# Performance work log

Hardware: AMD Instinct MI355X
Metric: run time of the kernel (lower is better)

## Reference

```python
import jax, jax.numpy as jnp
import numpy as np

N, G, C, CV, H = 2, 8, 64, 64, 2048
KA_ITERS = 2
EPS = 1e-20


def setup_inputs() -> dict:
    key = jax.random.key(0)
    k1, k2, k3 = jax.random.split(key, 3)
    q = jax.random.normal(k1, (N, G, C, H), dtype=jnp.float32)
    zeta = jax.random.normal(k2, (N, G, C, H), dtype=jnp.float32)
    mu = jax.random.normal(k3, (N, G, CV, H), dtype=jnp.float32)
    alpha = jnp.full((1,), 1.0 / np.sqrt(C), dtype=jnp.float32)  # uniform query precision
    beta = jnp.full((1,), 0.05, dtype=jnp.float32)               # uniform value precision
    return {"q": q, "zeta": zeta, "alpha": alpha, "mu": mu, "beta": beta}


def reference(q, zeta, alpha, mu, beta):
    # q, zeta: [N,G,C,H]; mu: [N,G,Cv,H]; alpha, beta: scalar (shape [1])
    a = alpha[0]
    b = beta[0]
    q2 = jnp.sum(q * q, axis=-2)      # [N,G,H]
    mu2 = jnp.sum(mu * mu, axis=-2)   # [N,G,H]

    def update_weights(zeta):
        z2 = jnp.sum(zeta * zeta, axis=-2)                     # [N,G,H]
        qz = jnp.einsum('bgci,bgcj->bgij', q, zeta)            # [N,G,H,H]
        # -0.5*alpha*||q_i - zeta_j||^2 (Mahalanobis with uniform precision)
        logp = -0.5 * a * (q2[..., :, None] + z2[..., None, :] - 2.0 * qz)
        # magnitude priors: + 0.5*alpha*||zeta_j||^2 + 0.5*beta*||mu_j||^2
        logp = logp + 0.5 * a * z2[..., None, :] + 0.5 * b * mu2[..., None, :]
        m = jnp.max(logp, axis=-1, keepdims=True)
        w = jnp.exp(logp - m)
        w = w / (jnp.sum(w, axis=-1, keepdims=True) + EPS)
        return w

    w = update_weights(zeta)
    for _ in range(KA_ITERS):
        # key adaptation (no zeta prior): zeta_j = sum_i w_ij q_i / sum_i w_ij
        zeta_upd = jnp.einsum('bgij,bgci->bgcj', w, q)         # [N,G,C,H]
        sum_w = jnp.sum(w, axis=-2, keepdims=True)             # [N,G,1,H]
        zeta = zeta_upd / sum_w
        w = update_weights(zeta)

    # value update: v_i = sum_j w_ij mu_j
    return jnp.einsum('bgij,bgcj->bgci', w, mu)                # [N,G,Cv,H]
```

## Files before the change

### kernel.cpp

```cpp
#include <hip/hip_runtime.h>

#define NB 16
#define CD 64
#define HD 2048

typedef unsigned short u16;
typedef __attribute__((ext_vector_type(8))) short s16x8;
typedef __attribute__((ext_vector_type(4))) float f32x4;

__device__ __forceinline__ u16 f2bf(float x){
    unsigned u = __float_as_uint(x);
    u += 0x7FFFu + ((u >> 16) & 1u);
    return (u16)(u >> 16);
}
__device__ __forceinline__ float bf2f(u16 h){ return __uint_as_float(((unsigned)h) << 16); }
__device__ __forceinline__ void split2(float x, u16& h, u16& l){
    h = f2bf(x); l = f2bf(x - bf2f(h));
}
union Frag { uint4 q; s16x8 s; };
__device__ __forceinline__ s16x8 ld8(const u16* p){ Frag f; f.q = *(const uint4*)p; return f.s; }
__device__ __forceinline__ f32x4 mfma16(s16x8 a, s16x8 b, f32x4 c){
    return __builtin_amdgcn_mfma_f32_16x16x32_bf16(a, b, c, 0, 0, 0);
}
__device__ __forceinline__ f32x4 mm2(s16x8 ah, s16x8 al, s16x8 bh, f32x4 c){
    c = mfma16(ah, bh, c);
    c = mfma16(al, bh, c);
    return c;
}
__device__ __forceinline__ f32x4 z4(){ f32x4 v = {0.f,0.f,0.f,0.f}; return v; }

__device__ __forceinline__ void xcd_map(int& bg, int& tile){
    int lb = blockIdx.y*32 + blockIdx.x;
    int xcd = lb & 7, t = lb >> 3;
    bg = 2*xcd + (t >> 5);
    tile = t & 31;
}


__global__ void k_convert(const float* __restrict__ src, u16* __restrict__ dh,
                          u16* __restrict__ dl, int n4)
{
    int idx = blockIdx.x*256 + threadIdx.x;
    if (idx >= n4) return;
    float4 v = ((const float4*)src)[idx];
    ushort4 h, l;
    split2(v.x, h.x, l.x); split2(v.y, h.y, l.y);
    split2(v.z, h.z, l.z); split2(v.w, h.w, l.w);
    ((ushort4*)dh)[idx] = h;
    ((ushort4*)dl)[idx] = l;
}

__global__ void k_convert1(const float* __restrict__ src, u16* __restrict__ dh, int n4)
{
    int idx = blockIdx.x*256 + threadIdx.x;
    if (idx >= n4) return;
    float4 v = ((const float4*)src)[idx];
    ushort4 h;
    h.x = f2bf(v.x); h.y = f2bf(v.y); h.z = f2bf(v.z); h.w = f2bf(v.w);
    ((ushort4*)dh)[idx] = h;
}

__global__ void k_transpose1(const float* __restrict__ src, u16* __restrict__ dh)
{
    int bg = blockIdx.y, h0 = blockIdx.x*128, tid = threadIdx.x;
    __shared__ float ft[CD][132];
    #pragma unroll
    for (int k=0;k<8;k++){
        int flat = tid + 256*k;
        int c = flat >> 5, p = (flat & 31)*4;
        *(float4*)&ft[c][p] = *(const float4*)(src + ((size_t)bg*CD + c)*HD + h0 + p);
    }
    __syncthreads();
    int hl = tid >> 1, c0 = (tid & 1)*32;
    union { u16 u[32]; uint4 q[4]; } oh;
    #pragma unroll
    for (int m=0;m<32;m++)
        oh.u[m] = f2bf(ft[c0+m][hl]);
    size_t base = ((size_t)bg*HD + h0 + hl)*CD + c0;
    #pragma unroll
    for (int t=0;t<4;t++)
        *((uint4*)(dh + base) + t) = oh.q[t];
}

__global__ void k_bias(const float* __restrict__ mu, const float* __restrict__ beta,
                       float* __restrict__ bias)
{
    int bg = blockIdx.y;
    int j  = blockIdx.x*256 + threadIdx.x;
    const float* m = mu + (size_t)bg*CD*HD + j;
    float s = 0.f;
    #pragma unroll
    for (int c=0;c<CD;c++){ float v = m[(size_t)c*HD]; s = fmaf(v, v, s); }
    bias[(size_t)bg*HD + j] = 0.5f * beta[0] * s;
}


__global__ __launch_bounds__(256,2) void k_rowsum(
    const u16* __restrict__ qTh,
    const u16* __restrict__ zTh,
    const float* __restrict__ bias, const float* __restrict__ alpha,
    float* __restrict__ r)
{
    int bg, itile; xcd_map(bg, itile);
    const int i0 = itile*64;
    const int tid = threadIdx.x, wave = tid>>6, lane = tid&63, ln = lane&15, quad = lane>>4;
    const int jw = wave*32;
    const float a = alpha[0];
    __shared__ float rpart[4][64];

    s16x8 Ah[4][2];
    #pragma unroll
    for (int mt=0;mt<4;mt++)
        #pragma unroll
        for (int ks=0;ks<2;ks++){
            size_t off = ((size_t)bg*HD + i0 + mt*16 + ln)*CD + ks*32 + quad*8;
            Ah[mt][ks] = ld8(qTh + off);
        }
    float racc[16];
    #pragma unroll
    for (int k=0;k<16;k++) racc[k] = 0.f;
    const float* bb = bias + (size_t)bg*HD;

    s16x8 B0h[2][2], B1h[2][2];
    float bj0[2], bj1[2];

    #pragma unroll
    for (int nt=0;nt<2;nt++){
        #pragma unroll
        for (int ks=0;ks<2;ks++){
            size_t off = ((size_t)bg*HD + jw + nt*16 + ln)*CD + ks*32 + quad*8;
            B0h[nt][ks] = ld8(zTh + off);
        }
        bj0[nt] = bb[jw + nt*16 + ln];
    }

    for (int j0=0;j0<HD;j0+=256){
        #pragma unroll
        for (int nt=0;nt<2;nt++){
            #pragma unroll
            for (int ks=0;ks<2;ks++){
                size_t off = ((size_t)bg*HD + j0+128 + jw + nt*16 + ln)*CD + ks*32 + quad*8;
                B1h[nt][ks] = ld8(zTh + off);
            }
            bj1[nt] = bb[j0+128 + jw + nt*16 + ln];
        }
        __builtin_amdgcn_sched_barrier(0);
        {
            f32x4 acc[4][2];
            #pragma unroll
            for (int mt=0;mt<4;mt++){ acc[mt][0]=z4(); acc[mt][1]=z4(); }
            __builtin_amdgcn_s_setprio(1);
            #pragma unroll
            for (int ks=0;ks<2;ks++)
                #pragma unroll
                for (int mt=0;mt<4;mt++)
                    #pragma unroll
                    for (int nt=0;nt<2;nt++)
                        acc[mt][nt] = mfma16(Ah[mt][ks], B0h[nt][ks], acc[mt][nt]);
            __builtin_amdgcn_s_setprio(0);
            #pragma unroll
            for (int mt=0;mt<4;mt++)
                #pragma unroll
                for (int nt=0;nt<2;nt++)
                    #pragma unroll
                    for (int rx=0;rx<4;rx++)
                        racc[mt*4+rx] += __expf(fmaf(a, acc[mt][nt][rx], bj0[nt]));
        }
        {
            int jn2 = (j0+256) & (HD-1);
            #pragma unroll
            for (int nt=0;nt<2;nt++){
                #pragma unroll
                for (int ks=0;ks<2;ks++){
                    size_t off = ((size_t)bg*HD + jn2 + jw + nt*16 + ln)*CD + ks*32 + quad*8;
                    B0h[nt][ks] = ld8(zTh + off);
                }
                bj0[nt] = bb[jn2 + jw + nt*16 + ln];
            }
        }
        __builtin_amdgcn_sched_barrier(0);
        {
            f32x4 acc[4][2];
            #pragma unroll
            for (int mt=0;mt<4;mt++){ acc[mt][0]=z4(); acc[mt][1]=z4(); }
            __builtin_amdgcn_s_setprio(1);
            #pragma unroll
            for (int ks=0;ks<2;ks++)
                #pragma unroll
                for (int mt=0;mt<4;mt++)
                    #pragma unroll
                    for (int nt=0;nt<2;nt++)
                        acc[mt][nt] = mfma16(Ah[mt][ks], B1h[nt][ks], acc[mt][nt]);
            __builtin_amdgcn_s_setprio(0);
            #pragma unroll
            for (int mt=0;mt<4;mt++)
                #pragma unroll
                for (int nt=0;nt<2;nt++)
                    #pragma unroll
                    for (int rx=0;rx<4;rx++)
                        racc[mt*4+rx] += __expf(fmaf(a, acc[mt][nt][rx], bj1[nt]));
        }
    }
    #pragma unroll
    for (int k=0;k<16;k++){
        float v = racc[k];
        v += __shfl_xor(v,1); v += __shfl_xor(v,2);
        v += __shfl_xor(v,4); v += __shfl_xor(v,8);
        racc[k] = v;
    }
    if (ln == 0){
        #pragma unroll
        for (int mt=0;mt<4;mt++)
            #pragma unroll
            for (int rx=0;rx<4;rx++)
                rpart[wave][mt*16 + quad*4 + rx] = racc[mt*4+rx];
    }
    __syncthreads();
    if (tid < 64)
        r[(size_t)bg*HD + i0 + tid] = rpart[0][tid]+rpart[1][tid]+rpart[2][tid]+rpart[3][tid];
}

__global__ __launch_bounds__(256,2) void k_update(
    const u16* __restrict__ qTh,
    u16* zTh,
    const u16* __restrict__ qNh,
    const float* __restrict__ bias, const float* __restrict__ alpha,
    const float* __restrict__ r)
{
    int bg, jtile; xcd_map(bg, jtile);
    const int j0 = jtile*64;
    const int tid = threadIdx.x, wave = tid>>6, lane = tid&63, ln = lane&15, quad = lane>>4;
    const int cm = (wave&1)*32, jn = (wave>>1)*32;
    const float a = alpha[0];
    __shared__ u16 wl[2][64*128];
    __shared__ float denl[4][64];

    s16x8 Bh[4][2];
    #pragma unroll
    for (int nt=0;nt<4;nt++)
        #pragma unroll
        for (int ks=0;ks<2;ks++){
            size_t off = ((size_t)bg*HD + j0 + nt*16 + ln)*CD + ks*32 + quad*8;
            Bh[nt][ks] = ld8(zTh + off);
        }
    float bj[4];
    #pragma unroll
    for (int nt=0;nt<4;nt++) bj[nt] = bias[(size_t)bg*HD + j0 + nt*16 + ln];

    f32x4 acc2[2][2] = {{z4(),z4()},{z4(),z4()}};
    float den[4] = {0.f,0.f,0.f,0.f};
    int buf = 0;

    for (int is=0; is<HD; is+=128, buf^=1){
        s16x8 Ah[2][2];
        #pragma unroll
        for (int ks=0;ks<2;ks++)
            #pragma unroll
            for (int mt=0;mt<2;mt++){
                size_t off = ((size_t)bg*HD + is + wave*32 + mt*16 + ln)*CD + ks*32 + quad*8;
                Ah[mt][ks] = ld8(qTh + off);
            }
        s16x8 A2h[4][2];
        #pragma unroll
        for (int ks2=0;ks2<4;ks2++)
            #pragma unroll
            for (int mtN=0;mtN<2;mtN++){
                size_t off = ((size_t)bg*CD + cm + mtN*16 + ln)*HD + is + ks2*32 + quad*8;
                A2h[ks2][mtN] = ld8(qNh + off);
            }
        float ri[8];
        #pragma unroll
        for (int mt=0;mt<2;mt++){
            float4 rv = *(const float4*)&r[(size_t)bg*HD + is + wave*32 + mt*16 + quad*4];
            ri[mt*4+0] = __builtin_amdgcn_rcpf(rv.x);
            ri[mt*4+1] = __builtin_amdgcn_rcpf(rv.y);
            ri[mt*4+2] = __builtin_amdgcn_rcpf(rv.z);
            ri[mt*4+3] = __builtin_amdgcn_rcpf(rv.w);
        }
        __builtin_amdgcn_sched_barrier(0);
        f32x4 acc1[2][4];
        #pragma unroll
        for (int mt=0;mt<2;mt++)
            #pragma unroll
            for (int nt=0;nt<4;nt++) acc1[mt][nt] = z4();
        __builtin_amdgcn_s_setprio(1);
        #pragma unroll
        for (int ks=0;ks<2;ks++)
            #pragma unroll
            for (int mt=0;mt<2;mt++)
                #pragma unroll
                for (int nt=0;nt<4;nt++)
                    acc1[mt][nt] = mfma16(Ah[mt][ks], Bh[nt][ks], acc1[mt][nt]);
        __builtin_amdgcn_s_setprio(0);
        #pragma unroll
        for (int mt=0;mt<2;mt++)
            #pragma unroll
            for (int nt=0;nt<4;nt++){
                u16 hh[4];
                #pragma unroll
                for (int rx=0;rx<4;rx++){
                    float w = __expf(fmaf(a, acc1[mt][nt][rx], bj[nt])) * ri[mt*4+rx];
                    hh[rx] = f2bf(w);
                    den[nt] += bf2f(hh[rx]);
                }
                int row = nt*16 + ln;
                int c4  = wave*32 + mt*16 + quad*4;
                int off = (row<<7) + ((((c4>>3) ^ (row&15))<<3) | (c4&7));
                *(ushort4*)&wl[buf][off] = make_ushort4(hh[0],hh[1],hh[2],hh[3]);
            }
        __syncthreads();
        __builtin_amdgcn_s_setprio(1);
        #pragma unroll
        for (int ks2=0;ks2<4;ks2++){
            s16x8 B2h[2];
            #pragma unroll
            for (int nt2=0;nt2<2;nt2++){
                int jl = jn + nt2*16 + ln;
                int ob = (jl<<7) + (((ks2*4+quad) ^ (jl&15))<<3);
                B2h[nt2] = ld8(&wl[buf][ob]);
            }
            #pragma unroll
            for (int mtN=0;mtN<2;mtN++)
                #pragma unroll
                for (int nt2=0;nt2<2;nt2++)
                    acc2[mtN][nt2] = mfma16(A2h[ks2][mtN], B2h[nt2], acc2[mtN][nt2]);
        }
        __builtin_amdgcn_s_setprio(0);
    }
    #pragma unroll
    for (int nt=0;nt<4;nt++){
        float v = den[nt];
        v += __shfl_xor(v,16); v += __shfl_xor(v,32);
        if (quad == 0) denl[wave][nt*16 + ln] = v;
    }
    __syncthreads();
    #pragma unroll
    for (int nt2=0;nt2<2;nt2++){
        int jl = jn + nt2*16 + ln;
        float dinv = __builtin_amdgcn_rcpf(denl[0][jl]+denl[1][jl]+denl[2][jl]+denl[3][jl]);
        #pragma unroll
        for (int mtN=0;mtN<2;mtN++){
            u16 hh[4];
            #pragma unroll
            for (int rx=0;rx<4;rx++)
                hh[rx] = f2bf(acc2[mtN][nt2][rx] * dinv);
            size_t off = ((size_t)bg*HD + j0 + jl)*CD + cm + mtN*16 + quad*4;
            *(ushort4*)(zTh + off) = make_ushort4(hh[0],hh[1],hh[2],hh[3]);
        }
    }
}

__global__ __launch_bounds__(256,2) void k_final(
    const u16* __restrict__ qTh,
    const u16* __restrict__ zTh,
    const u16* __restrict__ muh, const u16* __restrict__ mul_,
    const float* __restrict__ bias, const float* __restrict__ alpha,
    float* __restrict__ out)
{
    int bg, itile; xcd_map(bg, itile);
    const int i0 = itile*64;
    const int tid = threadIdx.x, wave = tid>>6, lane = tid&63, ln = lane&15, quad = lane>>4;
    const int cm = (wave&1)*32, in_ = (wave>>1)*32;
    const float a = alpha[0];
    __shared__ u16 el[2][64*128];
    __shared__ float rl2[4][64];

    s16x8 Bh[4][2];
    #pragma unroll
    for (int nt=0;nt<4;nt++)
        #pragma unroll
        for (int ks=0;ks<2;ks++){
            size_t off = ((size_t)bg*HD + i0 + nt*16 + ln)*CD + ks*32 + quad*8;
            Bh[nt][ks] = ld8(qTh + off);
        }
    f32x4 acc2[2][2] = {{z4(),z4()},{z4(),z4()}};
    float racc[4] = {0.f,0.f,0.f,0.f};
    int buf = 0;

    for (int js=0; js<HD; js+=128, buf^=1){
        s16x8 Ah[2][2];
        #pragma unroll
        for (int ks=0;ks<2;ks++)
            #pragma unroll
            for (int mt=0;mt<2;mt++){
                size_t off = ((size_t)bg*HD + js + wave*32 + mt*16 + ln)*CD + ks*32 + quad*8;
                Ah[mt][ks] = ld8(zTh + off);
            }
        s16x8 A2h[4][2], A2l[4][2];
        #pragma unroll
        for (int ks2=0;ks2<4;ks2++)
            #pragma unroll
            for (int mtN=0;mtN<2;mtN++){
                size_t off = ((size_t)bg*CD + cm + mtN*16 + ln)*HD + js + ks2*32 + quad*8;
                A2h[ks2][mtN] = ld8(muh + off);
                A2l[ks2][mtN] = ld8(mul_ + off);
            }
        float bj8[8];
        #pragma unroll
        for (int mt=0;mt<2;mt++){
            float4 bv = *(const float4*)&bias[(size_t)bg*HD + js + wave*32 + mt*16 + quad*4];
            bj8[mt*4+0]=bv.x; bj8[mt*4+1]=bv.y; bj8[mt*4+2]=bv.z; bj8[mt*4+3]=bv.w;
        }
        __builtin_amdgcn_sched_barrier(0);
        f32x4 acc1[2][4];
        #pragma unroll
        for (int mt=0;mt<2;mt++)
            #pragma unroll
            for (int nt=0;nt<4;nt++) acc1[mt][nt] = z4();
        __builtin_amdgcn_s_setprio(1);
        #pragma unroll
        for (int ks=0;ks<2;ks++)
            #pragma unroll
            for (int mt=0;mt<2;mt++)
                #pragma unroll
                for (int nt=0;nt<4;nt++)
                    acc1[mt][nt] = mfma16(Ah[mt][ks], Bh[nt][ks], acc1[mt][nt]);
        __builtin_amdgcn_s_setprio(0);
        #pragma unroll
        for (int mt=0;mt<2;mt++)
            #pragma unroll
            for (int nt=0;nt<4;nt++){
                u16 hh[4];
                #pragma unroll
                for (int rx=0;rx<4;rx++){
                    float e = __expf(fmaf(a, acc1[mt][nt][rx], bj8[mt*4+rx]));
                    hh[rx] = f2bf(e);
                    racc[nt] += bf2f(hh[rx]);
                }
                int row = nt*16 + ln;
                int c4  = wave*32 + mt*16 + quad*4;
                int off = (row<<7) + ((((c4>>3) ^ (row&15))<<3) | (c4&7));
                *(ushort4*)&el[buf][off] = make_ushort4(hh[0],hh[1],hh[2],hh[3]);
            }
        __syncthreads();
        __builtin_amdgcn_s_setprio(1);
        #pragma unroll
        for (int ks2=0;ks2<4;ks2++){
            s16x8 B2h[2];
            #pragma unroll
            for (int nt2=0;nt2<2;nt2++){
                int il = in_ + nt2*16 + ln;
                int ob = (il<<7) + (((ks2*4+quad) ^ (il&15))<<3);
                B2h[nt2] = ld8(&el[buf][ob]);
            }
            #pragma unroll
            for (int mtN=0;mtN<2;mtN++)
                #pragma unroll
                for (int nt2=0;nt2<2;nt2++)
                    acc2[mtN][nt2] = mm2(A2h[ks2][mtN], A2l[ks2][mtN], B2h[nt2], acc2[mtN][nt2]);
        }
        __builtin_amdgcn_s_setprio(0);
    }
    #pragma unroll
    for (int nt=0;nt<4;nt++){
        float v = racc[nt];
        v += __shfl_xor(v,16); v += __shfl_xor(v,32);
        if (quad == 0) rl2[wave][nt*16 + ln] = v;
    }
    __syncthreads();
    #pragma unroll
    for (int nt2=0;nt2<2;nt2++){
        int il = in_ + nt2*16 + ln;
        float rinv = __builtin_amdgcn_rcpf(rl2[0][il]+rl2[1][il]+rl2[2][il]+rl2[3][il]);
        #pragma unroll
        for (int mtN=0;mtN<2;mtN++)
            #pragma unroll
            for (int rx=0;rx<4;rx++)
                out[((size_t)bg*CD + cm + mtN*16 + quad*4 + rx)*HD + i0 + il]
                    = acc2[mtN][nt2][rx] * rinv;
    }
}

extern "C" void kernel_launch(void* const* d_in, const int* in_sizes, int n_in,
                              void* d_out, int out_size, void* d_ws, size_t ws_size,
                              hipStream_t stream)
{
    (void)in_sizes; (void)n_in; (void)out_size; (void)ws_size;
    const float* q     = (const float*)d_in[0];
    const float* zeta  = (const float*)d_in[1];
    const float* alpha = (const float*)d_in[2];
    const float* mu    = (const float*)d_in[3];
    const float* beta  = (const float*)d_in[4];
    float* out = (float*)d_out;

    const size_t SZ = (size_t)NB*HD*CD;
    u16* qTh = (u16*)d_ws;
    u16* zTh = qTh + 1*SZ;
    u16* qNh = qTh + 2*SZ;
    u16* muh = qTh + 3*SZ;
    u16* mul_= qTh + 4*SZ;
    float* bias = (float*)(qTh + 5*SZ);
    float* r    = bias + (size_t)NB*HD;

    dim3 blk(256,1,1);
    int n4 = (int)(SZ/4);
    k_convert1 <<<dim3(n4/256), blk, 0, stream>>>(q,  qNh, n4);
    k_convert  <<<dim3(n4/256), blk, 0, stream>>>(mu, muh, mul_, n4);
    k_transpose1<<<dim3(HD/128, NB), blk, 0, stream>>>(q,    qTh);
    k_transpose1<<<dim3(HD/128, NB), blk, 0, stream>>>(zeta, zTh);
    k_bias     <<<dim3(HD/256, NB), blk, 0, stream>>>(mu, beta, bias);

    k_rowsum<<<dim3(HD/64, NB), blk, 0, stream>>>(qTh,zTh,bias,alpha,r);
    k_update<<<dim3(HD/64, NB), blk, 0, stream>>>(qTh,zTh,qNh,bias,alpha,r);
    k_rowsum<<<dim3(HD/64, NB), blk, 0, stream>>>(qTh,zTh,bias,alpha,r);
    k_update<<<dim3(HD/64, NB), blk, 0, stream>>>(qTh,zTh,qNh,bias,alpha,r);
    k_final <<<dim3(HD/64, NB), blk, 0, stream>>>(qTh,zTh,muh,mul_,bias,alpha,out);
}
```

Before: 333.9 us.

## Software-pipeline global loads in update/final kernels and fuse q prep kernels

The k_update and k_final main loops are unrolled by two with ping-pong register sets, so the next tile's q/zeta fragments, reciprocals and bias loads are issued right after the current tile's first MFMA batch. This lets global-load latency hide behind the exp and second-GEMM work, where before it was exposed at the top of each iteration. Separately, the bf16 conversion of q and its transpose are merged into one kernel so q is read from global memory once. The cost is higher register pressure from the duplicated fragment buffers, which could lower occupancy.

```diff
diff --git a/kernel.cpp b/kernel.cpp
--- a/kernel.cpp
+++ b/kernel.cpp
@@ -50,14 +50,32 @@
     ((ushort4*)dl)[idx] = l;
 }
 
-__global__ void k_convert1(const float* __restrict__ src, u16* __restrict__ dh, int n4)
+__global__ void k_prep_q(const float* __restrict__ src, u16* __restrict__ dT,
+                         u16* __restrict__ dN)
 {
-    int idx = blockIdx.x*256 + threadIdx.x;
-    if (idx >= n4) return;
-    float4 v = ((const float4*)src)[idx];
-    ushort4 h;
-    h.x = f2bf(v.x); h.y = f2bf(v.y); h.z = f2bf(v.z); h.w = f2bf(v.w);
-    ((ushort4*)dh)[idx] = h;
+    int bg = blockIdx.y, h0 = blockIdx.x*128, tid = threadIdx.x;
+    __shared__ float ft[CD][132];
+    #pragma unroll
+    for (int k=0;k<8;k++){
+        int flat = tid + 256*k;
+        int c = flat >> 5, p = (flat & 31)*4;
+        size_t goff = ((size_t)bg*CD + c)*HD + h0 + p;
+        float4 v = *(const float4*)(src + goff);
+        *(float4*)&ft[c][p] = v;
+        ushort4 h;
+        h.x = f2bf(v.x); h.y = f2bf(v.y); h.z = f2bf(v.z); h.w = f2bf(v.w);
+        *(ushort4*)(dN + goff) = h;
+    }
+    __syncthreads();
+    int hl = tid >> 1, c0 = (tid & 1)*32;
+    union { u16 u[32]; uint4 q[4]; } oh;
+    #pragma unroll
+    for (int m=0;m<32;m++)
+        oh.u[m] = f2bf(ft[c0+m][hl]);
+    size_t base = ((size_t)bg*HD + h0 + hl)*CD + c0;
+    #pragma unroll
+    for (int t=0;t<4;t++)
+        *((uint4*)(dT + base) + t) = oh.q[t];
 }
 
 __global__ void k_transpose1(const float* __restrict__ src, u16* __restrict__ dh)
@@ -249,83 +267,185 @@
 
     f32x4 acc2[2][2] = {{z4(),z4()},{z4(),z4()}};
     float den[4] = {0.f,0.f,0.f,0.f};
-    int buf = 0;
-
-    for (int is=0; is<HD; is+=128, buf^=1){
-        s16x8 Ah[2][2];
-        #pragma unroll
-        for (int ks=0;ks<2;ks++)
+
+    s16x8 Ah0[2][2], A2h0[4][2]; float ri0[8];
+    s16x8 Ah1[2][2], A2h1[4][2]; float ri1[8];
+
+    #pragma unroll
+    for (int ks=0;ks<2;ks++)
+        #pragma unroll
+        for (int mt=0;mt<2;mt++){
+            size_t off = ((size_t)bg*HD + 0 + wave*32 + mt*16 + ln)*CD + ks*32 + quad*8;
+            Ah0[mt][ks] = ld8(qTh + off);
+        }
+    #pragma unroll
+    for (int ks2=0;ks2<4;ks2++)
+        #pragma unroll
+        for (int mtN=0;mtN<2;mtN++){
+            size_t off = ((size_t)bg*CD + cm + mtN*16 + ln)*HD + 0 + ks2*32 + quad*8;
+            A2h0[ks2][mtN] = ld8(qNh + off);
+        }
+    #pragma unroll
+    for (int mt=0;mt<2;mt++){
+        float4 rv = *(const float4*)&r[(size_t)bg*HD + 0 + wave*32 + mt*16 + quad*4];
+        ri0[mt*4+0] = __builtin_amdgcn_rcpf(rv.x);
+        ri0[mt*4+1] = __builtin_amdgcn_rcpf(rv.y);
+        ri0[mt*4+2] = __builtin_amdgcn_rcpf(rv.z);
+        ri0[mt*4+3] = __builtin_amdgcn_rcpf(rv.w);
+    }
+
+    for (int t=0; t<16; t+=2){
+        const int is1 = (t+1)*128, is2 = (t+2)*128;
+
+        {
+            f32x4 acc1[2][4];
+            #pragma unroll
+            for (int mt=0;mt<2;mt++)
+                #pragma unroll
+                for (int nt=0;nt<4;nt++) acc1[mt][nt] = z4();
+            __builtin_amdgcn_s_setprio(1);
+            #pragma unroll
+            for (int ks=0;ks<2;ks++)
+                #pragma unroll
+                for (int mt=0;mt<2;mt++)
+                    #pragma unroll
+                    for (int nt=0;nt<4;nt++)
+                        acc1[mt][nt] = mfma16(Ah0[mt][ks], Bh[nt][ks], acc1[mt][nt]);
+            __builtin_amdgcn_s_setprio(0);
+            #pragma unroll
+            for (int ks=0;ks<2;ks++)
+                #pragma unroll
+                for (int mt=0;mt<2;mt++){
+                    size_t off = ((size_t)bg*HD + is1 + wave*32 + mt*16 + ln)*CD + ks*32 + quad*8;
+                    Ah1[mt][ks] = ld8(qTh + off);
+                }
+            #pragma unroll
+            for (int ks2=0;ks2<4;ks2++)
+                #pragma unroll
+                for (int mtN=0;mtN<2;mtN++){
+                    size_t off = ((size_t)bg*CD + cm + mtN*16 + ln)*HD + is1 + ks2*32 + quad*8;
+                    A2h1[ks2][mtN] = ld8(qNh + off);
+                }
             #pragma unroll
             for (int mt=0;mt<2;mt++){
-                size_t off = ((size_t)bg*HD + is + wave*32 + mt*16 + ln)*CD + ks*32 + quad*8;
-                Ah[mt][ks] = ld8(qTh + off);
-            }
-        s16x8 A2h[4][2];
-        #pragma unroll
-        for (int ks2=0;ks2<4;ks2++)
-            #pragma unroll
-            for (int mtN=0;mtN<2;mtN++){
-                size_t off = ((size_t)bg*CD + cm + mtN*16 + ln)*HD + is + ks2*32 + quad*8;
-                A2h[ks2][mtN] = ld8(qNh + off);
-            }
-        float ri[8];
-        #pragma unroll
-        for (int mt=0;mt<2;mt++){
-            float4 rv = *(const float4*)&r[(size_t)bg*HD + is + wave*32 + mt*16 + quad*4];
-            ri[mt*4+0] = __builtin_amdgcn_rcpf(rv.x);
-            ri[mt*4+1] = __builtin_amdgcn_rcpf(rv.y);
-            ri[mt*4+2] = __builtin_amdgcn_rcpf(rv.z);
-            ri[mt*4+3] = __builtin_amdgcn_rcpf(rv.w);
-        }
-        __builtin_amdgcn_sched_barrier(0);
-        f32x4 acc1[2][4];
-        #pragma unroll
-        for (int mt=0;mt<2;mt++)
-            #pragma unroll
-            for (int nt=0;nt<4;nt++) acc1[mt][nt] = z4();
-        __builtin_amdgcn_s_setprio(1);
-        #pragma unroll
-        for (int ks=0;ks<2;ks++)
+                float4 rv = *(const float4*)&r[(size_t)bg*HD + is1 + wave*32 + mt*16 + quad*4];
+                ri1[mt*4+0] = __builtin_amdgcn_rcpf(rv.x);
+                ri1[mt*4+1] = __builtin_amdgcn_rcpf(rv.y);
+                ri1[mt*4+2] = __builtin_amdgcn_rcpf(rv.z);
+                ri1[mt*4+3] = __builtin_amdgcn_rcpf(rv.w);
+            }
+            __builtin_amdgcn_sched_barrier(0);
             #pragma unroll
             for (int mt=0;mt<2;mt++)
                 #pragma unroll
-                for (int nt=0;nt<4;nt++)
-                    acc1[mt][nt] = mfma16(Ah[mt][ks], Bh[nt][ks], acc1[mt][nt]);
-        __builtin_amdgcn_s_setprio(0);
-        #pragma unroll
-        for (int mt=0;mt<2;mt++)
-            #pragma unroll
-            for (int nt=0;nt<4;nt++){
-                u16 hh[4];
-                #pragma unroll
-                for (int rx=0;rx<4;rx++){
-                    float w = __expf(fmaf(a, acc1[mt][nt][rx], bj[nt])) * ri[mt*4+rx];
-                    hh[rx] = f2bf(w);
-                    den[nt] += bf2f(hh[rx]);
-                }
-                int row = nt*16 + ln;
-                int c4  = wave*32 + mt*16 + quad*4;
-                int off = (row<<7) + ((((c4>>3) ^ (row&15))<<3) | (c4&7));
-                *(ushort4*)&wl[buf][off] = make_ushort4(hh[0],hh[1],hh[2],hh[3]);
-            }
-        __syncthreads();
-        __builtin_amdgcn_s_setprio(1);
-        #pragma unroll
-        for (int ks2=0;ks2<4;ks2++){
-            s16x8 B2h[2];
-            #pragma unroll
-            for (int nt2=0;nt2<2;nt2++){
-                int jl = jn + nt2*16 + ln;
-                int ob = (jl<<7) + (((ks2*4+quad) ^ (jl&15))<<3);
-                B2h[nt2] = ld8(&wl[buf][ob]);
-            }
-            #pragma unroll
-            for (int mtN=0;mtN<2;mtN++)
-                #pragma unroll
-                for (int nt2=0;nt2<2;nt2++)
-                    acc2[mtN][nt2] = mfma16(A2h[ks2][mtN], B2h[nt2], acc2[mtN][nt2]);
-        }
-        __builtin_amdgcn_s_setprio(0);
+                for (int nt=0;nt<4;nt++){
+                    u16 hh[4];
+                    #pragma unroll
+                    for (int rx=0;rx<4;rx++){
+                        float w = __expf(fmaf(a, acc1[mt][nt][rx], bj[nt])) * ri0[mt*4+rx];
+                        hh[rx] = f2bf(w);
+                        den[nt] += bf2f(hh[rx]);
+                    }
+                    int row = nt*16 + ln;
+                    int c4  = wave*32 + mt*16 + quad*4;
+                    int off = (row<<7) + ((((c4>>3) ^ (row&15))<<3) | (c4&7));
+                    *(ushort4*)&wl[0][off] = make_ushort4(hh[0],hh[1],hh[2],hh[3]);
+                }
+            __syncthreads();
+            __builtin_amdgcn_s_setprio(1);
+            #pragma unroll
+            for (int ks2=0;ks2<4;ks2++){
+                s16x8 B2h[2];
+                #pragma unroll
+                for (int nt2=0;nt2<2;nt2++){
+                    int jl = jn + nt2*16 + ln;
+                    int ob = (jl<<7) + (((ks2*4+quad) ^ (jl&15))<<3);
+                    B2h[nt2] = ld8(&wl[0][ob]);
+                }
+                #pragma unroll
+                for (int mtN=0;mtN<2;mtN++)
+                    #pragma unroll
+                    for (int nt2=0;nt2<2;nt2++)
+                        acc2[mtN][nt2] = mfma16(A2h0[ks2][mtN], B2h[nt2], acc2[mtN][nt2]);
+            }
+            __builtin_amdgcn_s_setprio(0);
+        }
+
+        {
+            f32x4 acc1[2][4];
+            #pragma unroll
+            for (int mt=0;mt<2;mt++)
+                #pragma unroll
+                for (int nt=0;nt<4;nt++) acc1[mt][nt] = z4();
+            __builtin_amdgcn_s_setprio(1);
+            #pragma unroll
+            for (int ks=0;ks<2;ks++)
+                #pragma unroll
+                for (int mt=0;mt<2;mt++)
+                    #pragma unroll
+                    for (int nt=0;nt<4;nt++)
+                        acc1[mt][nt] = mfma16(Ah1[mt][ks], Bh[nt][ks], acc1[mt][nt]);
+            __builtin_amdgcn_s_setprio(0);
+            if (t < 14){
+                #pragma unroll
+                for (int ks=0;ks<2;ks++)
+                    #pragma unroll
+                    for (int mt=0;mt<2;mt++){
+                        size_t off = ((size_t)bg*HD + is2 + wave*32 + mt*16 + ln)*CD + ks*32 + quad*8;
+                        Ah0[mt][ks] = ld8(qTh + off);
+                    }
+                #pragma unroll
+                for (int ks2=0;ks2<4;ks2++)
+                    #pragma unroll
+                    for (int mtN=0;mtN<2;mtN++){
+                        size_t off = ((size_t)bg*CD + cm + mtN*16 + ln)*HD + is2 + ks2*32 + quad*8;
+                        A2h0[ks2][mtN] = ld8(qNh + off);
+                    }
+                #pragma unroll
+                for (int mt=0;mt<2;mt++){
+                    float4 rv = *(const float4*)&r[(size_t)bg*HD + is2 + wave*32 + mt*16 + quad*4];
+                    ri0[mt*4+0] = __builtin_amdgcn_rcpf(rv.x);
+                    ri0[mt*4+1] = __builtin_amdgcn_rcpf(rv.y);
+                    ri0[mt*4+2] = __builtin_amdgcn_rcpf(rv.z);
+                    ri0[mt*4+3] = __builtin_amdgcn_rcpf(rv.w);
+                }
+            }
+            __builtin_amdgcn_sched_barrier(0);
+            #pragma unroll
+            for (int mt=0;mt<2;mt++)
+                #pragma unroll
+                for (int nt=0;nt<4;nt++){
+                    u16 hh[4];
+                    #pragma unroll
+                    for (int rx=0;rx<4;rx++){
+                        float w = __expf(fmaf(a, acc1[mt][nt][rx], bj[nt])) * ri1[mt*4+rx];
+                        hh[rx] = f2bf(w);
+                        den[nt] += bf2f(hh[rx]);
+                    }
+                    int row = nt*16 + ln;
+                    int c4  = wave*32 + mt*16 + quad*4;
+                    int off = (row<<7) + ((((c4>>3) ^ (row&15))<<3) | (c4&7));
+                    *(ushort4*)&wl[1][off] = make_ushort4(hh[0],hh[1],hh[2],hh[3]);
+                }
+            __syncthreads();
+            __builtin_amdgcn_s_setprio(1);
+            #pragma unroll
+            for (int ks2=0;ks2<4;ks2++){
+                s16x8 B2h[2];
+                #pragma unroll
+                for (int nt2=0;nt2<2;nt2++){
+                    int jl = jn + nt2*16 + ln;
+                    int ob = (jl<<7) + (((ks2*4+quad) ^ (jl&15))<<3);
+                    B2h[nt2] = ld8(&wl[1][ob]);
+                }
+                #pragma unroll
+                for (int mtN=0;mtN<2;mtN++)
+                    #pragma unroll
+                    for (int nt2=0;nt2<2;nt2++)
+                        acc2[mtN][nt2] = mfma16(A2h1[ks2][mtN], B2h[nt2], acc2[mtN][nt2]);
+            }
+            __builtin_amdgcn_s_setprio(0);
+        }
     }
     #pragma unroll
     for (int nt=0;nt<4;nt++){
@@ -375,81 +495,173 @@
         }
     f32x4 acc2[2][2] = {{z4(),z4()},{z4(),z4()}};
     float racc[4] = {0.f,0.f,0.f,0.f};
-    int buf = 0;
-
-    for (int js=0; js<HD; js+=128, buf^=1){
-        s16x8 Ah[2][2];
-        #pragma unroll
-        for (int ks=0;ks<2;ks++)
+
+    s16x8 Ah0[2][2], Ah1[2][2];
+    float bj0[8], bj1[8];
+
+    #pragma unroll
+    for (int ks=0;ks<2;ks++)
+        #pragma unroll
+        for (int mt=0;mt<2;mt++){
+            size_t off = ((size_t)bg*HD + 0 + wave*32 + mt*16 + ln)*CD + ks*32 + quad*8;
+            Ah0[mt][ks] = ld8(zTh + off);
+        }
+    #pragma unroll
+    for (int mt=0;mt<2;mt++){
+        float4 bv = *(const float4*)&bias[(size_t)bg*HD + 0 + wave*32 + mt*16 + quad*4];
+        bj0[mt*4+0]=bv.x; bj0[mt*4+1]=bv.y; bj0[mt*4+2]=bv.z; bj0[mt*4+3]=bv.w;
+    }
+
+    for (int t=0; t<16; t+=2){
+        const int js0 = t*128, js1 = js0+128, js2 = js0+256;
+
+        {
+            s16x8 A2h[4][2], A2l[4][2];
+            #pragma unroll
+            for (int ks2=0;ks2<4;ks2++)
+                #pragma unroll
+                for (int mtN=0;mtN<2;mtN++){
+                    size_t off = ((size_t)bg*CD + cm + mtN*16 + ln)*HD + js0 + ks2*32 + quad*8;
+                    A2h[ks2][mtN] = ld8(muh + off);
+                    A2l[ks2][mtN] = ld8(mul_ + off);
+                }
+            f32x4 acc1[2][4];
+            #pragma unroll
+            for (int mt=0;mt<2;mt++)
+                #pragma unroll
+                for (int nt=0;nt<4;nt++) acc1[mt][nt] = z4();
+            __builtin_amdgcn_s_setprio(1);
+            #pragma unroll
+            for (int ks=0;ks<2;ks++)
+                #pragma unroll
+                for (int mt=0;mt<2;mt++)
+                    #pragma unroll
+                    for (int nt=0;nt<4;nt++)
+                        acc1[mt][nt] = mfma16(Ah0[mt][ks], Bh[nt][ks], acc1[mt][nt]);
+            __builtin_amdgcn_s_setprio(0);
+            #pragma unroll
+            for (int ks=0;ks<2;ks++)
+                #pragma unroll
+                for (int mt=0;mt<2;mt++){
+                    size_t off = ((size_t)bg*HD + js1 + wave*32 + mt*16 + ln)*CD + ks*32 + quad*8;
+                    Ah1[mt][ks] = ld8(zTh + off);
+                }
             #pragma unroll
             for (int mt=0;mt<2;mt++){
-                size_t off = ((size_t)bg*HD + js + wave*32 + mt*16 + ln)*CD + ks*32 + quad*8;
-                Ah[mt][ks] = ld8(zTh + off);
-            }
-        s16x8 A2h[4][2], A2l[4][2];
-        #pragma unroll
-        for (int ks2=0;ks2<4;ks2++)
-            #pragma unroll
-            for (int mtN=0;mtN<2;mtN++){
-                size_t off = ((size_t)bg*CD + cm + mtN*16 + ln)*HD + js + ks2*32 + quad*8;
-                A2h[ks2][mtN] = ld8(muh + off);
-                A2l[ks2][mtN] = ld8(mul_ + off);
-            }
-        float bj8[8];
-        #pragma unroll
-        for (int mt=0;mt<2;mt++){
-            float4 bv = *(const float4*)&bias[(size_t)bg*HD + js + wave*32 + mt*16 + quad*4];
-            bj8[mt*4+0]=bv.x; bj8[mt*4+1]=bv.y; bj8[mt*4+2]=bv.z; bj8[mt*4+3]=bv.w;
-        }
-        __builtin_amdgcn_sched_barrier(0);
-        f32x4 acc1[2][4];
-        #pragma unroll
-        for (int mt=0;mt<2;mt++)
-            #pragma unroll
-            for (int nt=0;nt<4;nt++) acc1[mt][nt] = z4();
-        __builtin_amdgcn_s_setprio(1);
-        #pragma unroll
-        for (int ks=0;ks<2;ks++)
+                float4 bv = *(const float4*)&bias[(size_t)bg*HD + js1 + wave*32 + mt*16 + quad*4];
+                bj1[mt*4+0]=bv.x; bj1[mt*4+1]=bv.y; bj1[mt*4+2]=bv.z; bj1[mt*4+3]=bv.w;
+            }
+            __builtin_amdgcn_sched_barrier(0);
             #pragma unroll
             for (int mt=0;mt<2;mt++)
                 #pragma unroll
-                for (int nt=0;nt<4;nt++)
-                    acc1[mt][nt] = mfma16(Ah[mt][ks], Bh[nt][ks], acc1[mt][nt]);
-        __builtin_amdgcn_s_setprio(0);
-        #pragma unroll
-        for (int mt=0;mt<2;mt++)
-            #pragma unroll
-            for (int nt=0;nt<4;nt++){
-                u16 hh[4];
-                #pragma unroll
-                for (int rx=0;rx<4;rx++){
-                    float e = __expf(fmaf(a, acc1[mt][nt][rx], bj8[mt*4+rx]));
-                    hh[rx] = f2bf(e);
-                    racc[nt] += bf2f(hh[rx]);
-                }
-                int row = nt*16 + ln;
-                int c4  = wave*32 + mt*16 + quad*4;
-                int off = (row<<7) + ((((c4>>3) ^ (row&15))<<3) | (c4&7));
-                *(ushort4*)&el[buf][off] = make_ushort4(hh[0],hh[1],hh[2],hh[3]);
-            }
-        __syncthreads();
-        __builtin_amdgcn_s_setprio(1);
-        #pragma unroll
-        for (int ks2=0;ks2<4;ks2++){
-            s16x8 B2h[2];
-            #pragma unroll
-            for (int nt2=0;nt2<2;nt2++){
-                int il = in_ + nt2*16 + ln;
-                int ob = (il<<7) + (((ks2*4+quad) ^ (il&15))<<3);
-                B2h[nt2] = ld8(&el[buf][ob]);
-            }
-            #pragma unroll
-            for (int mtN=0;mtN<2;mtN++)
-                #pragma unroll
-                for (int nt2=0;nt2<2;nt2++)
-                    acc2[mtN][nt2] = mm2(A2h[ks2][mtN], A2l[ks2][mtN], B2h[nt2], acc2[mtN][nt2]);
-        }
-        __builtin_amdgcn_s_setprio(0);
+                for (int nt=0;nt<4;nt++){
+                    u16 hh[4];
+                    #pragma unroll
+                    for (int rx=0;rx<4;rx++){
+                        float e = __expf(fmaf(a, acc1[mt][nt][rx], bj0[mt*4+rx]));
+                        hh[rx] = f2bf(e);
+                        racc[nt] += bf2f(hh[rx]);
+                    }
+                    int row = nt*16 + ln;
+                    int c4  = wave*32 + mt*16 + quad*4;
+                    int off = (row<<7) + ((((c4>>3) ^ (row&15))<<3) | (c4&7));
+                    *(ushort4*)&el[0][off] = make_ushort4(hh[0],hh[1],hh[2],hh[3]);
+                }
+            __syncthreads();
+            __builtin_amdgcn_s_setprio(1);
+            #pragma unroll
+            for (int ks2=0;ks2<4;ks2++){
+                s16x8 B2h[2];
+                #pragma unroll
+                for (int nt2=0;nt2<2;nt2++){
+                    int il = in_ + nt2*16 + ln;
+                    int ob = (il<<7) + (((ks2*4+quad) ^ (il&15))<<3);
+                    B2h[nt2] = ld8(&el[0][ob]);
+                }
+                #pragma unroll
+                for (int mtN=0;mtN<2;mtN++)
+                    #pragma unroll
+                    for (int nt2=0;nt2<2;nt2++)
+                        acc2[mtN][nt2] = mm2(A2h[ks2][mtN], A2l[ks2][mtN], B2h[nt2], acc2[mtN][nt2]);
+            }
+            __builtin_amdgcn_s_setprio(0);
+        }
+
+        {
+            s16x8 A2h[4][2], A2l[4][2];
+            #pragma unroll
+            for (int ks2=0;ks2<4;ks2++)
+                #pragma unroll
+                for (int mtN=0;mtN<2;mtN++){
+                    size_t off = ((size_t)bg*CD + cm + mtN*16 + ln)*HD + js1 + ks2*32 + quad*8;
+                    A2h[ks2][mtN] = ld8(muh + off);
+                    A2l[ks2][mtN] = ld8(mul_ + off);
+                }
+            f32x4 acc1[2][4];
+            #pragma unroll
+            for (int mt=0;mt<2;mt++)
+                #pragma unroll
+                for (int nt=0;nt<4;nt++) acc1[mt][nt] = z4();
+            __builtin_amdgcn_s_setprio(1);
+            #pragma unroll
+            for (int ks=0;ks<2;ks++)
+                #pragma unroll
+                for (int mt=0;mt<2;mt++)
+                    #pragma unroll
+                    for (int nt=0;nt<4;nt++)
+                        acc1[mt][nt] = mfma16(Ah1[mt][ks], Bh[nt][ks], acc1[mt][nt]);
+            __builtin_amdgcn_s_setprio(0);
+            if (t < 14){
+                #pragma unroll
+                for (int ks=0;ks<2;ks++)
+                    #pragma unroll
+                    for (int mt=0;mt<2;mt++){
+                        size_t off = ((size_t)bg*HD + js2 + wave*32 + mt*16 + ln)*CD + ks*32 + quad*8;
+                        Ah0[mt][ks] = ld8(zTh + off);
+                    }
+                #pragma unroll
+                for (int mt=0;mt<2;mt++){
+                    float4 bv = *(const float4*)&bias[(size_t)bg*HD + js2 + wave*32 + mt*16 + quad*4];
+                    bj0[mt*4+0]=bv.x; bj0[mt*4+1]=bv.y; bj0[mt*4+2]=bv.z; bj0[mt*4+3]=bv.w;
+                }
+            }
+            __builtin_amdgcn_sched_barrier(0);
+            #pragma unroll
+            for (int mt=0;mt<2;mt++)
+                #pragma unroll
+                for (int nt=0;nt<4;nt++){
+                    u16 hh[4];
+                    #pragma unroll
+                    for (int rx=0;rx<4;rx++){
+                        float e = __expf(fmaf(a, acc1[mt][nt][rx], bj1[mt*4+rx]));
+                        hh[rx] = f2bf(e);
+                        racc[nt] += bf2f(hh[rx]);
+                    }
+                    int row = nt*16 + ln;
+                    int c4  = wave*32 + mt*16 + quad*4;
+                    int off = (row<<7) + ((((c4>>3) ^ (row&15))<<3) | (c4&7));
+                    *(ushort4*)&el[1][off] = make_ushort4(hh[0],hh[1],hh[2],hh[3]);
+                }
+            __syncthreads();
+            __builtin_amdgcn_s_setprio(1);
+            #pragma unroll
+            for (int ks2=0;ks2<4;ks2++){
+                s16x8 B2h[2];
+                #pragma unroll
+                for (int nt2=0;nt2<2;nt2++){
+                    int il = in_ + nt2*16 + ln;
+                    int ob = (il<<7) + (((ks2*4+quad) ^ (il&15))<<3);
+                    B2h[nt2] = ld8(&el[1][ob]);
+                }
+                #pragma unroll
+                for (int mtN=0;mtN<2;mtN++)
+                    #pragma unroll
+                    for (int nt2=0;nt2<2;nt2++)
+                        acc2[mtN][nt2] = mm2(A2h[ks2][mtN], A2l[ks2][mtN], B2h[nt2], acc2[mtN][nt2]);
+            }
+            __builtin_amdgcn_s_setprio(0);
+        }
     }
     #pragma unroll
     for (int nt=0;nt<4;nt++){
@@ -494,9 +706,8 @@
 
     dim3 blk(256,1,1);
     int n4 = (int)(SZ/4);
-    k_convert1 <<<dim3(n4/256), blk, 0, stream>>>(q,  qNh, n4);
+    k_prep_q   <<<dim3(HD/128, NB), blk, 0, stream>>>(q, qTh, qNh);
     k_convert  <<<dim3(n4/256), blk, 0, stream>>>(mu, muh, mul_, n4);
-    k_transpose1<<<dim3(HD/128, NB), blk, 0, stream>>>(q,    qTh);
     k_transpose1<<<dim3(HD/128, NB), blk, 0, stream>>>(zeta, zTh);
     k_bias     <<<dim3(HD/256, NB), blk, 0, stream>>>(mu, beta, bias);
 
```

Measured after the change: 347.1 us. +3.9%, slower.

## Stage Q/Z key tiles through double-buffered swizzled LDS with register prefetch

Applied to the files above, without the earlier changes.

In k_update and k_final, the per-iteration A-operand tile (q or zeta, 128 rows by 64 channels) is now loaded from global memory with coalesced 16-byte loads. These loads are issued one iteration ahead and written into a double-buffered, XOR-swizzled LDS buffer after the barrier. Previously each wave loaded its fragments directly from global memory just before the first MFMA stage. The goal is to hide global latency behind the exp/softmax work and to make the loads coalesced. The cost is 32KB of extra LDS per block, which may reduce occupancy below the two blocks per CU targeted by the launch bounds, plus extra registers for the prefetch.

```diff
diff --git a/kernel.cpp b/kernel.cpp
--- a/kernel.cpp
+++ b/kernel.cpp
@@ -34,6 +34,10 @@
     int xcd = lb & 7, t = lb >> 3;
     bg = 2*xcd + (t >> 5);
     tile = t & 31;
+}
+
+__device__ __forceinline__ int stg_swz(int F){
+    return (F & ~127) | ((F & 127) ^ (((F >> 7) & 7) << 4));
 }
 
 
@@ -233,6 +237,7 @@
     const int cm = (wave&1)*32, jn = (wave>>1)*32;
     const float a = alpha[0];
     __shared__ u16 wl[2][64*128];
+    __shared__ u16 qs[2][128*64];
     __shared__ float denl[4][64];
 
     s16x8 Bh[4][2];
@@ -247,19 +252,21 @@
     #pragma unroll
     for (int nt=0;nt<4;nt++) bj[nt] = bias[(size_t)bg*HD + j0 + nt*16 + ln];
 
+    {
+        const u16* srcb = qTh + (size_t)bg*HD*CD;
+        #pragma unroll
+        for (int b=0;b<4;b++){
+            int F = wave*4096 + lane*16 + b*1024;
+            uint4 g = *(const uint4*)((const char*)srcb + F);
+            *(uint4*)&qs[0][stg_swz(F)>>1] = g;
+        }
+    }
+
     f32x4 acc2[2][2] = {{z4(),z4()},{z4(),z4()}};
     float den[4] = {0.f,0.f,0.f,0.f};
     int buf = 0;
 
     for (int is=0; is<HD; is+=128, buf^=1){
-        s16x8 Ah[2][2];
-        #pragma unroll
-        for (int ks=0;ks<2;ks++)
-            #pragma unroll
-            for (int mt=0;mt<2;mt++){
-                size_t off = ((size_t)bg*HD + is + wave*32 + mt*16 + ln)*CD + ks*32 + quad*8;
-                Ah[mt][ks] = ld8(qTh + off);
-            }
         s16x8 A2h[4][2];
         #pragma unroll
         for (int ks2=0;ks2<4;ks2++)
@@ -283,15 +290,38 @@
         for (int mt=0;mt<2;mt++)
             #pragma unroll
             for (int nt=0;nt<4;nt++) acc1[mt][nt] = z4();
-        __builtin_amdgcn_s_setprio(1);
-        #pragma unroll
-        for (int ks=0;ks<2;ks++)
-            #pragma unroll
-            for (int mt=0;mt<2;mt++)
-                #pragma unroll
-                for (int nt=0;nt<4;nt++)
-                    acc1[mt][nt] = mfma16(Ah[mt][ks], Bh[nt][ks], acc1[mt][nt]);
-        __builtin_amdgcn_s_setprio(0);
+        {
+            s16x8 Ah[2][2];
+            #pragma unroll
+            for (int ks=0;ks<2;ks++)
+                #pragma unroll
+                for (int mt=0;mt<2;mt++){
+                    int row = wave*32 + mt*16 + ln;
+                    int o   = ks*64 + quad*16;
+                    int ad  = row*128 + (o ^ ((row&7)<<4));
+                    Ah[mt][ks] = ld8(&qs[buf][ad>>1]);
+                }
+            __builtin_amdgcn_s_setprio(1);
+            #pragma unroll
+            for (int ks=0;ks<2;ks++)
+                #pragma unroll
+                for (int mt=0;mt<2;mt++)
+                    #pragma unroll
+                    for (int nt=0;nt<4;nt++)
+                        acc1[mt][nt] = mfma16(Ah[mt][ks], Bh[nt][ks], acc1[mt][nt]);
+            __builtin_amdgcn_s_setprio(0);
+        }
+        const bool st = (is + 128 < HD);
+        uint4 g0, g1, g2, g3;
+        if (st){
+            const char* srcb = (const char*)(qTh + ((size_t)bg*HD + is + 128)*CD);
+            int F = wave*4096 + lane*16;
+            g0 = *(const uint4*)(srcb + F);
+            g1 = *(const uint4*)(srcb + F + 1024);
+            g2 = *(const uint4*)(srcb + F + 2048);
+            g3 = *(const uint4*)(srcb + F + 3072);
+        }
+        __builtin_amdgcn_sched_barrier(0);
         #pragma unroll
         for (int mt=0;mt<2;mt++)
             #pragma unroll
@@ -309,6 +339,13 @@
                 *(ushort4*)&wl[buf][off] = make_ushort4(hh[0],hh[1],hh[2],hh[3]);
             }
         __syncthreads();
+        if (st){
+            int F = wave*4096 + lane*16;
+            *(uint4*)&qs[buf^1][stg_swz(F       )>>1] = g0;
+            *(uint4*)&qs[buf^1][stg_swz(F + 1024)>>1] = g1;
+            *(uint4*)&qs[buf^1][stg_swz(F + 2048)>>1] = g2;
+            *(uint4*)&qs[buf^1][stg_swz(F + 3072)>>1] = g3;
+        }
         __builtin_amdgcn_s_setprio(1);
         #pragma unroll
         for (int ks2=0;ks2<4;ks2++){
@@ -363,6 +400,7 @@
     const int cm = (wave&1)*32, in_ = (wave>>1)*32;
     const float a = alpha[0];
     __shared__ u16 el[2][64*128];
+    __shared__ u16 zs[2][128*64];
     __shared__ float rl2[4][64];
 
     s16x8 Bh[4][2];
@@ -373,19 +411,20 @@
             size_t off = ((size_t)bg*HD + i0 + nt*16 + ln)*CD + ks*32 + quad*8;
             Bh[nt][ks] = ld8(qTh + off);
         }
+    {
+        const u16* srcb = zTh + (size_t)bg*HD*CD;
+        #pragma unroll
+        for (int b=0;b<4;b++){
+            int F = wave*4096 + lane*16 + b*1024;
+            uint4 g = *(const uint4*)((const char*)srcb + F);
+            *(uint4*)&zs[0][stg_swz(F)>>1] = g;
+        }
+    }
     f32x4 acc2[2][2] = {{z4(),z4()},{z4(),z4()}};
     float racc[4] = {0.f,0.f,0.f,0.f};
     int buf = 0;
 
     for (int js=0; js<HD; js+=128, buf^=1){
-        s16x8 Ah[2][2];
-        #pragma unroll
-        for (int ks=0;ks<2;ks++)
-            #pragma unroll
-            for (int mt=0;mt<2;mt++){
-                size_t off = ((size_t)bg*HD + js + wave*32 + mt*16 + ln)*CD + ks*32 + quad*8;
-                Ah[mt][ks] = ld8(zTh + off);
-            }
         s16x8 A2h[4][2], A2l[4][2];
         #pragma unroll
         for (int ks2=0;ks2<4;ks2++)
@@ -407,15 +446,38 @@
         for (int mt=0;mt<2;mt++)
             #pragma unroll
             for (int nt=0;nt<4;nt++) acc1[mt][nt] = z4();
-        __builtin_amdgcn_s_setprio(1);
-        #pragma unroll
-        for (int ks=0;ks<2;ks++)
-            #pragma unroll
-            for (int mt=0;mt<2;mt++)
-                #pragma unroll
-                for (int nt=0;nt<4;nt++)
-                    acc1[mt][nt] = mfma16(Ah[mt][ks], Bh[nt][ks], acc1[mt][nt]);
-        __builtin_amdgcn_s_setprio(0);
+        {
+            s16x8 Ah[2][2];
+            #pragma unroll
+            for (int ks=0;ks<2;ks++)
+                #pragma unroll
+                for (int mt=0;mt<2;mt++){
+                    int row = wave*32 + mt*16 + ln;
+                    int o   = ks*64 + quad*16;
+                    int ad  = row*128 + (o ^ ((row&7)<<4));
+                    Ah[mt][ks] = ld8(&zs[buf][ad>>1]);
+                }
+            __builtin_amdgcn_s_setprio(1);
+            #pragma unroll
+            for (int ks=0;ks<2;ks++)
+                #pragma unroll
+                for (int mt=0;mt<2;mt++)
+                    #pragma unroll
+                    for (int nt=0;nt<4;nt++)
+                        acc1[mt][nt] = mfma16(Ah[mt][ks], Bh[nt][ks], acc1[mt][nt]);
+            __builtin_amdgcn_s_setprio(0);
+        }
+        const bool st = (js + 128 < HD);
+        uint4 g0, g1, g2, g3;
+        if (st){
+            const char* srcb = (const char*)(zTh + ((size_t)bg*HD + js + 128)*CD);
+            int F = wave*4096 + lane*16;
+            g0 = *(const uint4*)(srcb + F);
+            g1 = *(const uint4*)(srcb + F + 1024);
+            g2 = *(const uint4*)(srcb + F + 2048);
+            g3 = *(const uint4*)(srcb + F + 3072);
+        }
+        __builtin_amdgcn_sched_barrier(0);
         #pragma unroll
         for (int mt=0;mt<2;mt++)
             #pragma unroll
@@ -433,6 +495,13 @@
                 *(ushort4*)&el[buf][off] = make_ushort4(hh[0],hh[1],hh[2],hh[3]);
             }
         __syncthreads();
+        if (st){
+            int F = wave*4096 + lane*16;
+            *(uint4*)&zs[buf^1][stg_swz(F       )>>1] = g0;
+            *(uint4*)&zs[buf^1][stg_swz(F + 1024)>>1] = g1;
+            *(uint4*)&zs[buf^1][stg_swz(F + 2048)>>1] = g2;
+            *(uint4*)&zs[buf^1][stg_swz(F + 3072)>>1] = g3;
+        }
         __builtin_amdgcn_s_setprio(1);
         #pragma unroll
         for (int ks2=0;ks2<4;ks2++){
```

Measured after the change: 303.5 us. -9.1%, faster.
